# Performance work log

Measured on AMD Instinct MI355X. Metric: run time of the kernel, lower is better.

## Reference

```python
import jax, jax.numpy as jnp
import numpy as np

KERNEL_SIGMA2 = 4096.0  # = 2 * x_dim, assumed Gaussian RBF kernel

B, K, D, H, Z = 512, 32, 2048, 512, 64


def setup_inputs() -> dict:
    key = jax.random.key(0)
    ks = jax.random.split(key, 8)
    s = lambda k, shp, fan: jax.random.normal(k, shp, jnp.float32) / np.sqrt(fan)
    return {
        "x_c": jax.random.normal(ks[0], (B, D), jnp.float32),
        "x_nn": jax.random.normal(ks[1], (B, K, D), jnp.float32),
        "W1": s(ks[2], (D, H), D), "b1": jnp.zeros((H,), jnp.float32),
        "W2": s(ks[3], (H, Z), H), "b2": jnp.zeros((Z,), jnp.float32),
        "V1": s(ks[4], (Z, H), Z), "c1": jnp.zeros((H,), jnp.float32),
        "V2": s(ks[5], (H, D), H), "c2": jnp.zeros((D,), jnp.float32),
    }


def _enc(x, W1, b1, W2, b2):
    return jax.nn.relu(x @ W1 + b1) @ W2 + b2


def _dec(z, V1, c1, V2, c2):
    return jax.nn.relu(z @ V1 + c1) @ V2 + c2


def reference(x_c, x_nn, W1, b1, W2, b2, V1, c1, V2, c2):
    bs, num_nn, x_dim = x_nn.shape
    z_c = _enc(x_c, W1, b1, W2, b2)                       # [B, Z]
    z_dim = z_c.shape[1]
    z_nn = _enc(x_nn.reshape(bs * num_nn, x_dim), W1, b1, W2, b2)
    z_nn = z_nn.reshape(bs, num_nn, z_dim)
    dz = z_nn - z_c[:, None, :]                           # [B, K, Z]

    # first-order Taylor: recon(z_c) + J(z_c) @ dz via JVP of decoder
    dec_fn = lambda z: _dec(z, V1, c1, V2, c2)
    inputs = jnp.broadcast_to(z_c[:, None, :], (bs, num_nn, z_dim)).reshape(-1, z_dim)
    _, Jdz = jax.jvp(dec_fn, (inputs,), (dz.reshape(-1, z_dim),))  # [B*K, D]

    recon = dec_fn(z_c)                                   # [B, D]
    n_recon = recon[:, None, :] + Jdz.reshape(bs, num_nn, x_dim)

    diff = x_nn - n_recon
    n_loss = jnp.sum(diff * diff, axis=2)                 # ||.||^2, [B, K]
    w = jnp.exp(-jnp.sum((x_nn - x_c[:, None, :]) ** 2, axis=2) / KERNEL_SIGMA2)
    return jnp.mean(w * n_loss)
```

## Files before the change

### kernel.cpp

```cpp
#include <hip/hip_runtime.h>
#include <hip/hip_bf16.h>
#include <cstdint>
#include <cstddef>

#define DEV __device__ __forceinline__

typedef __bf16 bf16;
typedef __bf16 bf16x8 __attribute__((ext_vector_type(8)));
typedef float f32x4 __attribute__((ext_vector_type(4)));

DEV f32x4 mfma16(bf16x8 a, bf16x8 b, f32x4 c) {
  return __builtin_amdgcn_mfma_f32_16x16x32_bf16(a, b, c, 0, 0, 0);
}

DEV void glds16(const void* g, void* l) {
  __builtin_amdgcn_global_load_lds(
      (const __attribute__((address_space(1))) void*)g,
      (__attribute__((address_space(3))) void*)l, 16, 0, 0);
}

template<int ROWS, int NT>
DEV void stage_tile(const bf16* __restrict__ src, int ld, int row0, int k0,
                    unsigned char* lds, int tid) {
  constexpr int CALLS = (ROWS * 128) / (NT * 16);
  const int wid = tid >> 6, lane = tid & 63;
#pragma unroll
  for (int c = 0; c < CALLS; ++c) {
    const int obase = c * (NT * 16) + wid * 1024;
    const int o = obase + lane * 16;
    const int row = o >> 7;
    const int scb = (o & 127) ^ ((row & 7) << 4);
    glds16(src + (size_t)(row0 + row) * ld + k0 + (scb >> 1), lds + obase);
  }
}

template<int ROWS, int NT>
DEV void stage_tile_f32(const float* __restrict__ src, int ld, int row0, int k0,
                        unsigned char* lds, int tid) {
  constexpr int CALLS = (ROWS * 256) / (NT * 16);
  const int wid = tid >> 6, lane = tid & 63;
#pragma unroll
  for (int c = 0; c < CALLS; ++c) {
    const int obase = c * (NT * 16) + wid * 1024;
    const int o = obase + lane * 16;
    const int row = o >> 8;
    const int scb = (o & 255) ^ ((row & 7) << 4);
    glds16(src + (size_t)(row0 + row) * ld + k0 + (scb >> 2), lds + obase);
  }
}

template<int BM, int BN, int WM, int WN, int MODE, int AF32, int MINW = 2>
__global__ __launch_bounds__(WM*WN*64, MINW) void gemm_kernel(
    const bf16* __restrict__ A, const float* __restrict__ Af,
    const float* __restrict__ Af2,
    const bf16* __restrict__ Bt, const float* __restrict__ bias,
    int M, int N, int K,
    float* __restrict__ out32, bf16* __restrict__ out16,
    const float* __restrict__ hc, const float* __restrict__ recon,
    float* __restrict__ nloss, float* __restrict__ warg)
{
  constexpr int NT = WM * WN * 64;
  constexpr int FM = (BM / WM) / 16;
  constexpr int FN = (BN / WN) / 16;
  constexpr int HALF = (BM + BN) * 128;
  __shared__ __align__(16) unsigned char smem[AF32 ? (BM * 256 + BN * 128) : HALF];

  const int tid = threadIdx.x, lane = tid & 63, wid = tid >> 6;
  const int wm = wid / WN, wn = wid % WN;
  const int wm0 = wm * (BM / WM), wn0 = wn * (BN / WN);

  int bx = blockIdx.x, by = blockIdx.y;
  {
    const int gx = gridDim.x;
    const int nwg = gx * gridDim.y;
    if ((nwg & 7) == 0) {
      const int fid = by * gx + bx;
      const int cpx = nwg >> 3;
      const int w = (fid & 7) * cpx + (fid >> 3);
      bx = w % gx; by = w / gx;
    }
  }
  const int i0 = by * BM, j0 = bx * BN;
  const int l15 = lane & 15, lg = lane >> 4;

  f32x4 acc[FM][FN] = {};

  int arow[FM], brow[FN];
#pragma unroll
  for (int mi = 0; mi < FM; ++mi) arow[mi] = wm0 + mi * 16 + l15;
#pragma unroll
  for (int ni = 0; ni < FN; ++ni) brow[ni] = wn0 + ni * 16 + l15;

  auto compute = [&](const unsigned char* cA, const unsigned char* cB) {
#pragma unroll
    for (int kh = 0; kh < 2; ++kh) {
      bf16x8 af[FM], bfr[FN];
      if constexpr (AF32) {
        const int Fb = kh * 128 + lg * 32;
#pragma unroll
        for (int mi = 0; mi < FM; ++mi) {
          const int r = arow[mi];
          const unsigned char* p = cA + r * 256;
          const f32x4 lo = *reinterpret_cast<const f32x4*>(p + ((Fb)      ^ ((r & 7) << 4)));
          const f32x4 hi = *reinterpret_cast<const f32x4*>(p + ((Fb + 16) ^ ((r & 7) << 4)));
          bf16x8 a;
          a[0] = (bf16)lo[0]; a[1] = (bf16)lo[1]; a[2] = (bf16)lo[2]; a[3] = (bf16)lo[3];
          a[4] = (bf16)hi[0]; a[5] = (bf16)hi[1]; a[6] = (bf16)hi[2]; a[7] = (bf16)hi[3];
          af[mi] = a;
        }
      } else {
        const int koff = kh * 64 + lg * 16;
#pragma unroll
        for (int mi = 0; mi < FM; ++mi) {
          const int off = (arow[mi] * 128 + koff) ^ ((arow[mi] & 7) << 4);
          af[mi] = *reinterpret_cast<const bf16x8*>(cA + off);
        }
      }
      const int koffB = kh * 64 + lg * 16;
#pragma unroll
      for (int ni = 0; ni < FN; ++ni) {
        const int off = (brow[ni] * 128 + koffB) ^ ((brow[ni] & 7) << 4);
        bfr[ni] = *reinterpret_cast<const bf16x8*>(cB + off);
      }
#pragma unroll
      for (int mi = 0; mi < FM; ++mi)
#pragma unroll
        for (int ni = 0; ni < FN; ++ni)
          acc[mi][ni] = mfma16(af[mi], bfr[ni], acc[mi][ni]);
    }
  };

  if constexpr (AF32) {
    const float* As = (i0 < 512) ? Af + (size_t)i0 * K
                                 : Af2 + (size_t)(i0 - 512) * K;
    for (int kt = 0; kt < K; kt += 64) {
      stage_tile_f32<BM, NT>(As, K, 0, kt, smem, tid);
      stage_tile<BN, NT>(Bt, K, j0, kt, smem + BM * 256, tid);
      __syncthreads();
      compute(smem, smem + BM * 256);
      __syncthreads();
    }
  } else {
    for (int kt = 0; kt < K; kt += 64) {
      stage_tile<BM, NT>(A, K, i0, kt, smem, tid);
      stage_tile<BN, NT>(Bt, K, j0, kt, smem + BM * 128, tid);
      __syncthreads();
      compute(smem, smem + BM * 128);
      __syncthreads();
    }
  }

  if constexpr (MODE == 5) {
    float* eb = (float*)smem;
#pragma unroll
    for (int mi = 0; mi < FM; ++mi) {
      __syncthreads();
#pragma unroll
      for (int ni = 0; ni < FN; ++ni) {
        const int col = wn0 + ni * 16 + l15;
        const int lr0 = wm * 16 + lg * 4;
#pragma unroll
        for (int r = 0; r < 4; ++r)
          eb[(lr0 + r) * 132 + col] = acc[mi][ni][r];
      }
      __syncthreads();
      const int lrow = tid >> 3;
      const int c0 = (tid & 7) * 16;
      const int grow = i0 + (lrow >> 4) * 64 + mi * 16 + (lrow & 15);
      const int b = grow >> 5;
      const float* xp = Af2  + (size_t)grow * 2048 + j0 + c0;
      const float* cp = Af   + (size_t)b * 2048 + j0 + c0;
      const float* rp = recon + (size_t)b * 2048 + j0 + c0;
      float nl = 0.f, wa = 0.f;
#pragma unroll
      for (int q4 = 0; q4 < 4; ++q4) {
        const float4 xv = *(const float4*)(xp + q4 * 4);
        const float4 cv = *(const float4*)(cp + q4 * 4);
        const float4 rv = *(const float4*)(rp + q4 * 4);
#pragma unroll
        for (int q = 0; q < 4; ++q) {
          const float xf = ((const float*)&xv)[q];
          const float d = xf - ((const float*)&rv)[q] - eb[lrow * 132 + c0 + q4 * 4 + q];
          nl += d * d;
          const float wd = xf - ((const float*)&cv)[q];
          wa += wd * wd;
        }
      }
      nl += __shfl_xor(nl, 1, 64); wa += __shfl_xor(wa, 1, 64);
      nl += __shfl_xor(nl, 2, 64); wa += __shfl_xor(wa, 2, 64);
      nl += __shfl_xor(nl, 4, 64); wa += __shfl_xor(wa, 4, 64);
      if ((tid & 7) == 0) {
        atomicAdd(&nloss[grow], nl);
        atomicAdd(&warg[grow], wa);
      }
    }
  } else {
#pragma unroll
    for (int mi = 0; mi < FM; ++mi) {
#pragma unroll
      for (int ni = 0; ni < FN; ++ni) {
#pragma unroll
        for (int r = 0; r < 4; ++r) {
          const int row = i0 + wm0 + mi * 16 + lg * 4 + r;
          const int col = j0 + wn0 + ni * 16 + l15;
          float v = acc[mi][ni][r];
          if constexpr (MODE == 0) {
            v += bias[col];
            out16[(size_t)row * N + col] = (bf16)fmaxf(v, 0.f);
          } else if constexpr (MODE == 1) {
            v += bias[col];
            out32[(size_t)row * N + col] = v;
          } else if constexpr (MODE == 2) {
            v += bias[col];
            out32[(size_t)row * N + col] = v;
            out16[(size_t)row * N + col] = (bf16)fmaxf(v, 0.f);
          } else if constexpr (MODE == 4) {
            const int b = row >> 5;
            const float m = hc[(size_t)b * 512 + col];
            out16[(size_t)row * N + col] = (bf16)(m > 0.f ? v : 0.f);
          }
        }
      }
    }
  }
}

__global__ void transpose_all_kernel(
    const float* __restrict__ W1, const float* __restrict__ W2,
    const float* __restrict__ V1, const float* __restrict__ V2,
    bf16* __restrict__ W1t, bf16* __restrict__ W2t,
    bf16* __restrict__ V1t, bf16* __restrict__ V2t) {
  int blk = blockIdx.x;
  const float* src; bf16* dst; int R, C, gx;
  if (blk < 1024)      { src = W1; dst = W1t; R = 2048; C = 512;  gx = 16; }
  else if (blk < 1056) { blk -= 1024; src = W2; dst = W2t; R = 512; C = 64;   gx = 2;  }
  else if (blk < 1088) { blk -= 1056; src = V1; dst = V1t; R = 64;  C = 512;  gx = 16; }
  else                 { blk -= 1088; src = V2; dst = V2t; R = 512; C = 2048; gx = 64; }
  __shared__ float t[32][33];
  const int c0 = (blk % gx) * 32, r0 = (blk / gx) * 32;
  const int tx = threadIdx.x, ty = threadIdx.y;
#pragma unroll
  for (int i = 0; i < 32; i += 8)
    t[ty + i][tx] = src[(size_t)(r0 + ty + i) * C + c0 + tx];
  __syncthreads();
#pragma unroll
  for (int i = 0; i < 32; i += 8)
    dst[(size_t)(c0 + ty + i) * R + r0 + tx] = (bf16)t[tx][ty + i];
}

__global__ void dz_prep_kernel(const float* __restrict__ z,
                               bf16* __restrict__ dzb,
                               bf16* __restrict__ zcb,
                               float* __restrict__ nw,
                               float* __restrict__ out) {
  const int i = blockIdx.x * 256 + threadIdx.x;
  if (i < 32768) nw[i] = 0.f;
  if (i == 0) out[0] = 0.f;
  const int r = i >> 6, j = i & 63;
  const float v = z[i];
  if (r < 512) {
    zcb[i] = (bf16)v;
  } else {
    const int rn = r - 512;
    const int b = rn >> 5;
    dzb[(size_t)rn * 64 + j] = (bf16)(v - z[(size_t)b * 64 + j]);
  }
}

__global__ void finalize_kernel(const float* __restrict__ nloss,
                                const float* __restrict__ warg,
                                float* __restrict__ out) {
  const int i = blockIdx.x * 256 + threadIdx.x;
  float v = expf(-warg[i] * (1.0f / 4096.0f)) * nloss[i] * (1.0f / 16384.0f);
#pragma unroll
  for (int s = 1; s < 64; s <<= 1) v += __shfl_xor(v, s, 64);
  __shared__ float red[4];
  const int lane = threadIdx.x & 63, w = threadIdx.x >> 6;
  if (lane == 0) red[w] = v;
  __syncthreads();
  if (threadIdx.x == 0) atomicAdd(out, red[0] + red[1] + red[2] + red[3]);
}

extern "C" void kernel_launch(void* const* d_in, const int* in_sizes, int n_in,
                              void* d_out, int out_size, void* d_ws, size_t ws_size,
                              hipStream_t stream) {
  const float* x_c = (const float*)d_in[0];
  const float* x_nn = (const float*)d_in[1];
  const float* W1 = (const float*)d_in[2];
  const float* b1 = (const float*)d_in[3];
  const float* W2 = (const float*)d_in[4];
  const float* b2 = (const float*)d_in[5];
  const float* V1 = (const float*)d_in[6];
  const float* c1 = (const float*)d_in[7];
  const float* V2 = (const float*)d_in[8];
  const float* c2 = (const float*)d_in[9];
  float* out = (float*)d_out;
  char* ws = (char*)d_ws;

  size_t off = 0;
  auto take = [&](size_t n) { size_t o = off; off += n; return o; };
  bf16*  W1t   = (bf16*) (ws + take((size_t)512 * 2048 * 2));
  bf16*  W2t   = (bf16*) (ws + take((size_t)64 * 512 * 2));
  bf16*  V1t   = (bf16*) (ws + take((size_t)512 * 64 * 2));
  bf16*  V2t   = (bf16*) (ws + take((size_t)2048 * 512 * 2));
  bf16*  h1    = (bf16*) (ws + take((size_t)16896 * 512 * 2));
  float* z     = (float*)(ws + take((size_t)16896 * 64 * 4));
  bf16*  dzb   = (bf16*) (ws + take((size_t)16384 * 64 * 2));
  bf16*  zcb   = (bf16*) (ws + take((size_t)512 * 64 * 2));
  float* hc    = (float*)(ws + take((size_t)512 * 512 * 4));
  bf16*  acb   = (bf16*) (ws + take((size_t)512 * 512 * 2));
  float* recon = (float*)(ws + take((size_t)512 * 2048 * 4));
  bf16*  dab   = (bf16*) (ws + take((size_t)16384 * 512 * 2));
  float* nloss = (float*)(ws + take((size_t)16384 * 4));
  float* warg  = (float*)(ws + take((size_t)16384 * 4));

  transpose_all_kernel<<<dim3(2112), dim3(32, 8), 0, stream>>>(
      W1, W2, V1, V2, W1t, W2t, V1t, V2t);

  gemm_kernel<64, 128, 2, 2, 0, 1><<<dim3(4, 264), dim3(256), 0, stream>>>(
      nullptr, x_c, x_nn, W1t, b1, 16896, 512, 2048,
      nullptr, h1, nullptr, nullptr, nullptr, nullptr);

  gemm_kernel<64, 64, 2, 2, 1, 0><<<dim3(1, 264), dim3(256), 0, stream>>>(
      h1, nullptr, nullptr, W2t, b2, 16896, 64, 512,
      z, nullptr, nullptr, nullptr, nullptr, nullptr);

  dz_prep_kernel<<<dim3(4224), dim3(256), 0, stream>>>(z, dzb, zcb, nloss, out);

  gemm_kernel<128, 128, 2, 2, 2, 0><<<dim3(4, 4), dim3(256), 0, stream>>>(
      zcb, nullptr, nullptr, V1t, c1, 512, 512, 64,
      hc, acb, nullptr, nullptr, nullptr, nullptr);

  gemm_kernel<64, 128, 2, 2, 1, 0><<<dim3(16, 8), dim3(256), 0, stream>>>(
      acb, nullptr, nullptr, V2t, c2, 512, 2048, 512,
      recon, nullptr, nullptr, nullptr, nullptr, nullptr);

  gemm_kernel<128, 128, 2, 2, 4, 0><<<dim3(4, 128), dim3(256), 0, stream>>>(
      dzb, nullptr, nullptr, V1t, nullptr, 16384, 512, 64,
      nullptr, dab, hc, nullptr, nullptr, nullptr);

  gemm_kernel<128, 128, 2, 2, 5, 0><<<dim3(16, 128), dim3(256), 0, stream>>>(
      dab, x_c, x_nn, V2t, nullptr, 16384, 2048, 512,
      nullptr, nullptr, nullptr, recon, nloss, warg);

  finalize_kernel<<<dim3(64), dim3(256), 0, stream>>>(nloss, warg, out);
}
```

Baseline: 168.6 us.

## Pre-cast inputs to bf16 and use bf16 A-path with larger tiles in first GEMM

Adds a separate kernel that converts x_c and x_nn from fp32 to a bf16 buffer. The first encoder GEMM then stages bf16 A tiles instead of fp32 tiles and converting them in registers, and its tile grows from 64x128 to 128x128. The fp32-A template path is removed. The cost is an extra full pass over x (about 138MB read, 69MB written) before the GEMM, which in exchange reads half the A bytes per tile, does no per-fragment conversions, and gets more reuse from the larger tile.

```diff
diff --git a/kernel.cpp b/kernel.cpp
--- a/kernel.cpp
+++ b/kernel.cpp
@@ -34,22 +34,7 @@
   }
 }
 
-template<int ROWS, int NT>
-DEV void stage_tile_f32(const float* __restrict__ src, int ld, int row0, int k0,
-                        unsigned char* lds, int tid) {
-  constexpr int CALLS = (ROWS * 256) / (NT * 16);
-  const int wid = tid >> 6, lane = tid & 63;
-#pragma unroll
-  for (int c = 0; c < CALLS; ++c) {
-    const int obase = c * (NT * 16) + wid * 1024;
-    const int o = obase + lane * 16;
-    const int row = o >> 8;
-    const int scb = (o & 255) ^ ((row & 7) << 4);
-    glds16(src + (size_t)(row0 + row) * ld + k0 + (scb >> 2), lds + obase);
-  }
-}
-
-template<int BM, int BN, int WM, int WN, int MODE, int AF32, int MINW = 2>
+template<int BM, int BN, int WM, int WN, int MODE, int MINW = 2>
 __global__ __launch_bounds__(WM*WN*64, MINW) void gemm_kernel(
     const bf16* __restrict__ A, const float* __restrict__ Af,
     const float* __restrict__ Af2,
@@ -62,8 +47,7 @@
   constexpr int NT = WM * WN * 64;
   constexpr int FM = (BM / WM) / 16;
   constexpr int FN = (BN / WN) / 16;
-  constexpr int HALF = (BM + BN) * 128;
-  __shared__ __align__(16) unsigned char smem[AF32 ? (BM * 256 + BN * 128) : HALF];
+  __shared__ __align__(16) unsigned char smem[(BM + BN) * 128];
 
   const int tid = threadIdx.x, lane = tid & 63, wid = tid >> 6;
   const int wm = wid / WN, wn = wid % WN;
@@ -94,32 +78,16 @@
   auto compute = [&](const unsigned char* cA, const unsigned char* cB) {
 #pragma unroll
     for (int kh = 0; kh < 2; ++kh) {
+      const int koff = kh * 64 + lg * 16;
       bf16x8 af[FM], bfr[FN];
-      if constexpr (AF32) {
-        const int Fb = kh * 128 + lg * 32;
-#pragma unroll
-        for (int mi = 0; mi < FM; ++mi) {
-          const int r = arow[mi];
-          const unsigned char* p = cA + r * 256;
-          const f32x4 lo = *reinterpret_cast<const f32x4*>(p + ((Fb)      ^ ((r & 7) << 4)));
-          const f32x4 hi = *reinterpret_cast<const f32x4*>(p + ((Fb + 16) ^ ((r & 7) << 4)));
-          bf16x8 a;
-          a[0] = (bf16)lo[0]; a[1] = (bf16)lo[1]; a[2] = (bf16)lo[2]; a[3] = (bf16)lo[3];
-          a[4] = (bf16)hi[0]; a[5] = (bf16)hi[1]; a[6] = (bf16)hi[2]; a[7] = (bf16)hi[3];
-          af[mi] = a;
-        }
-      } else {
-        const int koff = kh * 64 + lg * 16;
-#pragma unroll
-        for (int mi = 0; mi < FM; ++mi) {
-          const int off = (arow[mi] * 128 + koff) ^ ((arow[mi] & 7) << 4);
-          af[mi] = *reinterpret_cast<const bf16x8*>(cA + off);
-        }
-      }
-      const int koffB = kh * 64 + lg * 16;
+#pragma unroll
+      for (int mi = 0; mi < FM; ++mi) {
+        const int off = (arow[mi] * 128 + koff) ^ ((arow[mi] & 7) << 4);
+        af[mi] = *reinterpret_cast<const bf16x8*>(cA + off);
+      }
 #pragma unroll
       for (int ni = 0; ni < FN; ++ni) {
-        const int off = (brow[ni] * 128 + koffB) ^ ((brow[ni] & 7) << 4);
+        const int off = (brow[ni] * 128 + koff) ^ ((brow[ni] & 7) << 4);
         bfr[ni] = *reinterpret_cast<const bf16x8*>(cB + off);
       }
 #pragma unroll
@@ -130,24 +98,12 @@
     }
   };
 
-  if constexpr (AF32) {
-    const float* As = (i0 < 512) ? Af + (size_t)i0 * K
-                                 : Af2 + (size_t)(i0 - 512) * K;
-    for (int kt = 0; kt < K; kt += 64) {
-      stage_tile_f32<BM, NT>(As, K, 0, kt, smem, tid);
-      stage_tile<BN, NT>(Bt, K, j0, kt, smem + BM * 256, tid);
-      __syncthreads();
-      compute(smem, smem + BM * 256);
-      __syncthreads();
-    }
-  } else {
-    for (int kt = 0; kt < K; kt += 64) {
-      stage_tile<BM, NT>(A, K, i0, kt, smem, tid);
-      stage_tile<BN, NT>(Bt, K, j0, kt, smem + BM * 128, tid);
-      __syncthreads();
-      compute(smem, smem + BM * 128);
-      __syncthreads();
-    }
+  for (int kt = 0; kt < K; kt += 64) {
+    stage_tile<BM, NT>(A, K, i0, kt, smem, tid);
+    stage_tile<BN, NT>(Bt, K, j0, kt, smem + BM * 128, tid);
+    __syncthreads();
+    compute(smem, smem + BM * 128);
+    __syncthreads();
   }
 
   if constexpr (MODE == 5) {
@@ -225,6 +181,20 @@
   }
 }
 
+__global__ void cast_x_kernel(const float* __restrict__ x_c,
+                              const float* __restrict__ x_nn,
+                              bf16* __restrict__ xb) {
+  const size_t i = ((size_t)blockIdx.x * 256 + threadIdx.x) * 8;
+  constexpr size_t XC = (size_t)512 * 2048;
+  const float* s = (i < XC) ? x_c + i : x_nn + (i - XC);
+  const float4 a = *(const float4*)s;
+  const float4 b = *(const float4*)(s + 4);
+  bf16x8 v;
+  v[0] = (bf16)a.x; v[1] = (bf16)a.y; v[2] = (bf16)a.z; v[3] = (bf16)a.w;
+  v[4] = (bf16)b.x; v[5] = (bf16)b.y; v[6] = (bf16)b.z; v[7] = (bf16)b.w;
+  *(bf16x8*)(xb + i) = v;
+}
+
 __global__ void transpose_all_kernel(
     const float* __restrict__ W1, const float* __restrict__ W2,
     const float* __restrict__ V1, const float* __restrict__ V2,
@@ -313,33 +283,36 @@
   bf16*  dab   = (bf16*) (ws + take((size_t)16384 * 512 * 2));
   float* nloss = (float*)(ws + take((size_t)16384 * 4));
   float* warg  = (float*)(ws + take((size_t)16384 * 4));
+  bf16*  xb    = (bf16*) (ws + take((size_t)16896 * 2048 * 2));
+
+  cast_x_kernel<<<dim3(16896), dim3(256), 0, stream>>>(x_c, x_nn, xb);
 
   transpose_all_kernel<<<dim3(2112), dim3(32, 8), 0, stream>>>(
       W1, W2, V1, V2, W1t, W2t, V1t, V2t);
 
-  gemm_kernel<64, 128, 2, 2, 0, 1><<<dim3(4, 264), dim3(256), 0, stream>>>(
-      nullptr, x_c, x_nn, W1t, b1, 16896, 512, 2048,
+  gemm_kernel<128, 128, 2, 2, 0><<<dim3(4, 132), dim3(256), 0, stream>>>(
+      xb, nullptr, nullptr, W1t, b1, 16896, 512, 2048,
       nullptr, h1, nullptr, nullptr, nullptr, nullptr);
 
-  gemm_kernel<64, 64, 2, 2, 1, 0><<<dim3(1, 264), dim3(256), 0, stream>>>(
+  gemm_kernel<64, 64, 2, 2, 1><<<dim3(1, 264), dim3(256), 0, stream>>>(
       h1, nullptr, nullptr, W2t, b2, 16896, 64, 512,
       z, nullptr, nullptr, nullptr, nullptr, nullptr);
 
   dz_prep_kernel<<<dim3(4224), dim3(256), 0, stream>>>(z, dzb, zcb, nloss, out);
 
-  gemm_kernel<128, 128, 2, 2, 2, 0><<<dim3(4, 4), dim3(256), 0, stream>>>(
+  gemm_kernel<128, 128, 2, 2, 2><<<dim3(4, 4), dim3(256), 0, stream>>>(
       zcb, nullptr, nullptr, V1t, c1, 512, 512, 64,
       hc, acb, nullptr, nullptr, nullptr, nullptr);
 
-  gemm_kernel<64, 128, 2, 2, 1, 0><<<dim3(16, 8), dim3(256), 0, stream>>>(
+  gemm_kernel<64, 128, 2, 2, 1><<<dim3(16, 8), dim3(256), 0, stream>>>(
       acb, nullptr, nullptr, V2t, c2, 512, 2048, 512,
       recon, nullptr, nullptr, nullptr, nullptr, nullptr);
 
-  gemm_kernel<128, 128, 2, 2, 4, 0><<<dim3(4, 128), dim3(256), 0, stream>>>(
+  gemm_kernel<128, 128, 2, 2, 4><<<dim3(4, 128), dim3(256), 0, stream>>>(
       dzb, nullptr, nullptr, V1t, nullptr, 16384, 512, 64,
       nullptr, dab, hc, nullptr, nullptr, nullptr);
 
-  gemm_kernel<128, 128, 2, 2, 5, 0><<<dim3(16, 128), dim3(256), 0, stream>>>(
+  gemm_kernel<128, 128, 2, 2, 5><<<dim3(16, 128), dim3(256), 0, stream>>>(
       dab, x_c, x_nn, V2t, nullptr, 16384, 2048, 512,
       nullptr, nullptr, nullptr, recon, nloss, warg);
 
```

Result: slower. 173.7 us (+3.0%).
